# Optimization experiments

Measured on AMD Instinct MI355X. Metric: run time of the kernel, lower is better.

The kernel has to match this reference:

```python
import jax, jax.numpy as jnp
import numpy as np

B, S, E, NH = 2, 2048, 1024, 16
THETA = 10000.0


def setup_inputs() -> dict:
    key = jax.random.key(0)
    k1, k2 = jax.random.split(key, 2)
    hidden_states = jax.random.normal(k1, (B, S, E), dtype=jnp.float32)
    in_proj_weight = jax.random.normal(k2, (3 * E, E), dtype=jnp.float32) * 0.02
    in_proj_bias = jnp.zeros((3 * E,), dtype=jnp.float32)
    return {
        "hidden_states": hidden_states,
        "in_proj_weight": in_proj_weight,
        "in_proj_bias": in_proj_bias,
        "T": 1,
        "H": 32,
        "W": 64,
    }


def _rope(x, cos, sin):
    # x: [BT, seq, n_heads, head_dim]; cos/sin: [seq, head_dim//2]
    # pairs are consecutive elements (x[2i], x[2i+1]) == complex (re, im)
    xr = x.reshape(x.shape[:-1] + (-1, 2))
    xe, xo = xr[..., 0], xr[..., 1]
    c = cos[None, :, None, :]
    s = sin[None, :, None, :]
    re = xe * c - xo * s
    im = xe * s + xo * c
    return jnp.stack([re, im], axis=-1).reshape(x.shape)


def reference(hidden_states, in_proj_weight, in_proj_bias, T, H, W):
    Bx, Sx, Ex = hidden_states.shape
    hd = Ex // NH
    # fused QKV projection
    qkv = hidden_states @ in_proj_weight.T + in_proj_bias
    q, k, v = jnp.split(qkv, 3, axis=-1)
    # 1D rotary over chunks of length S//T (T=1 -> full sequence)
    seq = Sx // T
    inv_freq = 1.0 / (THETA ** (jnp.arange(0, hd, 2, dtype=jnp.float32) / hd))
    ang = jnp.arange(seq, dtype=jnp.float32)[:, None] * inv_freq  # [seq, hd//2]
    cos, sin = jnp.cos(ang), jnp.sin(ang)
    q = _rope(q.reshape(Bx * T, seq, NH, hd), cos, sin).reshape(Bx, Sx, NH, hd)
    k = _rope(k.reshape(Bx * T, seq, NH, hd), cos, sin).reshape(Bx, Sx, NH, hd)
    v = v.reshape(Bx, Sx, NH, hd)
    # scaled dot-product attention (special_attn encoder path: no out_proj)
    scale = 1.0 / jnp.sqrt(jnp.asarray(hd, dtype=jnp.float32))
    scores = jnp.einsum('bqnd,bknd->bnqk', q, k) * scale
    attn = jax.nn.softmax(scores, axis=-1)
    out = jnp.einsum('bnqk,bknd->bqnd', attn, v)
    return out.reshape(Bx, Sx, Ex)
```

## Files before the change

kernel.cpp:

```cpp
#include <hip/hip_runtime.h>
#include <math.h>

#define BB 2
#define SS 2048
#define EE 1024
#define NHH 16
#define HD 64
#define HD2 32

typedef _Float16 f16x8 __attribute__((ext_vector_type(8)));
typedef __attribute__((ext_vector_type(4))) float f32x4;

static __device__ __forceinline__ unsigned pkh(float a, float b) {
    union { _Float16 h[2]; unsigned u; } v;
    v.h[0] = (_Float16)a; v.h[1] = (_Float16)b;
    return v.u;
}

static __device__ __forceinline__ void dma16(const void* g, void* l) {
    __builtin_amdgcn_global_load_lds(
        (const __attribute__((address_space(1))) unsigned int*)g,
        (__attribute__((address_space(3))) unsigned int*)l,
        16, 0, 0);
}

__global__ __launch_bounds__(256) void rope_table_k(float* __restrict__ ct,
                                                    float* __restrict__ st) {
    int idx = blockIdx.x * 256 + threadIdx.x;
    if (idx >= SS * HD2) return;
    int s = idx >> 5, p = idx & 31;
    double inv = pow(10000.0, -(double)(2 * p) / 64.0);
    double ang = (double)s * inv;
    ct[idx] = (float)cos(ang);
    st[idx] = (float)sin(ang);
}

#define NXCHUNK 524288
#define NWCHUNK 393216
__global__ __launch_bounds__(256) void cvt_k(
    const float* __restrict__ X, const float* __restrict__ W,
    unsigned short* __restrict__ Xh, unsigned short* __restrict__ Wh)
{
    int idx = blockIdx.x * 256 + threadIdx.x;
    const float* src;
    unsigned short* dst;
    int c;
    if (idx < NXCHUNK) { src = X; dst = Xh; c = idx; }
    else               { src = W; dst = Wh; c = idx - NXCHUNK;
                         if (c >= NWCHUNK) return; }
    int l15 = c & 15, q = (c >> 4) & 3, grp = (c >> 6) & 7;
    int kt = (c >> 9) & 31, t = c >> 14;
    int row = t * 128 + grp * 16 + l15;
    int k   = kt * 32 + q * 8;
    float4 v0 = *(const float4*)(src + (size_t)row * EE + k);
    float4 v1 = *(const float4*)(src + (size_t)row * EE + k + 4);
    *(uint4*)(dst + (size_t)c * 8) =
        make_uint4(pkh(v0.x, v0.y), pkh(v0.z, v0.w), pkh(v1.x, v1.y), pkh(v1.z, v1.w));
}

__global__ __launch_bounds__(256, 3) void qkv_mfma_k(
    const unsigned short* __restrict__ Xh, const unsigned short* __restrict__ Wh,
    const float* __restrict__ bias,
    const float* __restrict__ ct, const float* __restrict__ st,
    unsigned short* __restrict__ Qg, unsigned short* __restrict__ Kg,
    unsigned short* __restrict__ Vg)
{
    __shared__ __align__(16) unsigned short Alds[4096];
    __shared__ __align__(16) unsigned short Blds[4096];

    const int tid  = threadIdx.x;
    const int wave = tid >> 6;
    const int lane = tid & 63;
    const int quad = lane >> 4;
    const int l15  = lane & 15;

    const int id    = blockIdx.x;
    const int xcd   = id & 7;
    const int local = id >> 3;
    const int nt    = xcd * 3 + local % 3;
    const int mt    = local / 3;
    const int m0    = mt * 128;
    const int n0b   = nt * 128;

    f32x4 acc[4][4];
#pragma unroll
    for (int mc = 0; mc < 4; mc++)
#pragma unroll
        for (int nc = 0; nc < 4; nc++) acc[mc][nc] = (f32x4){0.f, 0.f, 0.f, 0.f};

    const int mg = (wave >> 1) * 4;
    const int ng = (wave & 1) * 4;

    for (int kt = 0; kt < EE / 32; kt++) {
        __syncthreads();
        {
            const unsigned short* at = Xh + ((size_t)(mt * 32 + kt)) * 4096;
            const unsigned short* bt = Wh + ((size_t)(nt * 32 + kt)) * 4096;
            dma16(at + (size_t)tid * 8,         Alds + tid * 8);
            dma16(at + (size_t)(tid + 256) * 8, Alds + (tid + 256) * 8);
            dma16(bt + (size_t)tid * 8,         Blds + tid * 8);
            dma16(bt + (size_t)(tid + 256) * 8, Blds + (tid + 256) * 8);
        }
        __syncthreads();

        f16x8 Af[4], Bf[4];
#pragma unroll
        for (int mc = 0; mc < 4; mc++)
            Af[mc] = *(const f16x8*)(Alds + ((mg + mc) * 4 + quad) * 128 + l15 * 8);
#pragma unroll
        for (int nc = 0; nc < 4; nc++)
            Bf[nc] = *(const f16x8*)(Blds + ((ng + nc) * 4 + quad) * 128 + l15 * 8);
#pragma unroll
        for (int mc = 0; mc < 4; mc++)
#pragma unroll
            for (int nc = 0; nc < 4; nc++)
                acc[mc][nc] = __builtin_amdgcn_mfma_f32_16x16x32_f16(Af[mc], Bf[nc], acc[mc][nc], 0, 0, 0);
    }

    const int n0w = n0b + (wave & 1) * 64;
    const int m0w = m0 + (wave >> 1) * 64;
    const int sec = n0w >> 10;
    const int h   = (n0w & 1023) >> 6;
    const int bq  = m0w >> 11;
    const size_t abase = (size_t)(bq * NHH + h) * 131072;
    unsigned short* dst = (sec == 0) ? Qg : (sec == 1) ? Kg : Vg;

    float bn[4];
#pragma unroll
    for (int nc = 0; nc < 4; nc++) bn[nc] = bias[n0w + nc * 16 + l15];

    if (sec < 2) {
        const float scq = (sec == 0) ? 0.18033688f : 1.0f;
#pragma unroll
        for (int mc = 0; mc < 4; mc++) {
            int sb = (m0w & 2047) + mc * 16;
#pragma unroll
            for (int nc = 0; nc < 4; nc++) {
                int d = nc * 16 + l15;
                int p = d >> 1;
                int kc_d = d >> 5, quad_a = (d >> 3) & 3, j = d & 7;
#pragma unroll
                for (int rr = 0; rr < 4; rr++) {
                    int srow = sb + quad * 4 + rr;
                    float x = acc[mc][nc][rr] + bn[nc];
                    float xp = __shfl_xor(x, 1);
                    float c = ct[srow * 32 + p], sn = st[srow * 32 + p];
                    float o = ((l15 & 1) == 0) ? (x * c - xp * sn) : (xp * sn + x * c);
                    o *= scq;
                    float op = __shfl_xor(o, 1);
                    if ((l15 & 1) == 0) {
                        unsigned u = pkh(o, op);
                        size_t e = abase +
                            (size_t)((((srow >> 4) * 2 + kc_d) * 4 + quad_a)) * 128 +
                            (srow & 15) * 8 + j;
                        *(unsigned int*)(dst + e) = u;
                    }
                }
            }
        }
    } else {
#pragma unroll
        for (int mc = 0; mc < 4; mc++) {
            int sb = (m0w & 2047) + mc * 16;
            int s32 = sb >> 5;
            int quad_v = ((sb >> 3) + (quad >> 1)) & 3;
            int j0 = (quad & 1) * 4;
#pragma unroll
            for (int nc = 0; nc < 4; nc++) {
                float x0 = acc[mc][nc][0] + bn[nc];
                float x1 = acc[mc][nc][1] + bn[nc];
                float x2 = acc[mc][nc][2] + bn[nc];
                float x3 = acc[mc][nc][3] + bn[nc];
                unsigned u01 = pkh(x0, x1), u23 = pkh(x2, x3);
                size_t e = abase +
                    (size_t)(((s32 * 4 + nc) * 4 + quad_v)) * 128 + l15 * 8 + j0;
                *(uint2*)(dst + e) = make_uint2(u01, u23);
            }
        }
    }
}

__global__ __launch_bounds__(256, 4) void attn_mfma_k(
    const unsigned short* __restrict__ Qg,
    const unsigned short* __restrict__ Kg,
    const unsigned short* __restrict__ Vg,
    float* __restrict__ out)
{
    __shared__ __align__(16) unsigned short Klds[2][4096];
    __shared__ __align__(16) unsigned short Pbuf[4][1024];

    const int tid  = threadIdx.x;
    const int wave = tid >> 6;
    const int lane = tid & 63;
    const int quad = lane >> 4;
    const int l15  = lane & 15;
    const int id   = blockIdx.x;
    const int bh   = (id & 7) * 4 + ((id >> 3) & 3);
    const int qt   = id >> 5;
    const int b    = bh >> 4, h = bh & 15;
    const int q0   = qt * 64 + wave * 16;
    const size_t abase = (size_t)bh * 131072;

    f16x8 qf[2];
#pragma unroll
    for (int kc = 0; kc < 2; kc++)
        qf[kc] = *(const f16x8*)(Qg + abase +
            (size_t)((((q0 >> 4) * 2 + kc) * 4 + quad)) * 128 + l15 * 8);

    f32x4 acc[4];
#pragma unroll
    for (int dc = 0; dc < 4; dc++) acc[dc] = (f32x4){0.f, 0.f, 0.f, 0.f};
    float mst = -INFINITY, lst = 0.f;

    const unsigned short* kgb = Kg + abase;
    const unsigned short* vgb = Vg + abase;
    unsigned short* Pw = Pbuf[wave];

    dma16(kgb + (size_t)tid * 8,         &Klds[0][tid * 8]);
    dma16(kgb + (size_t)(tid + 256) * 8, &Klds[0][(tid + 256) * 8]);
    __syncthreads();

    int cur = 0;
    for (int kt = 0; kt < SS / 64; kt++) {
        if (kt + 1 < SS / 64) {
            const unsigned short* ks = kgb + (size_t)(kt + 1) * 4096;
            dma16(ks + (size_t)tid * 8,         &Klds[cur ^ 1][tid * 8]);
            dma16(ks + (size_t)(tid + 256) * 8, &Klds[cur ^ 1][(tid + 256) * 8]);
        }

        const unsigned short* vt = vgb + (size_t)kt * 4096;
        f16x8 vf[4][2];
#pragma unroll
        for (int dc = 0; dc < 4; dc++)
#pragma unroll
            for (int kk2 = 0; kk2 < 2; kk2++)
                vf[dc][kk2] = *(const f16x8*)(vt + (kk2 * 16 + dc * 4 + quad) * 128 + l15 * 8);

        f32x4 stt[4];
        __builtin_amdgcn_s_setprio(1);
#pragma unroll
        for (int mc = 0; mc < 4; mc++) {
            f16x8 a0 = *(const f16x8*)(&Klds[cur][((mc * 2 + 0) * 4 + quad) * 128 + l15 * 8]);
            f16x8 a1 = *(const f16x8*)(&Klds[cur][((mc * 2 + 1) * 4 + quad) * 128 + l15 * 8]);
            f32x4 s = (f32x4){0.f, 0.f, 0.f, 0.f};
            s = __builtin_amdgcn_mfma_f32_16x16x32_f16(a0, qf[0], s, 0, 0, 0);
            s = __builtin_amdgcn_mfma_f32_16x16x32_f16(a1, qf[1], s, 0, 0, 0);
            stt[mc] = s;
        }
        __builtin_amdgcn_s_setprio(0);

        float mt = -INFINITY;
#pragma unroll
        for (int mc = 0; mc < 4; mc++)
#pragma unroll
            for (int rr = 0; rr < 4; rr++) mt = fmaxf(mt, stt[mc][rr]);
        mt = fmaxf(mt, __shfl_xor(mt, 16));
        mt = fmaxf(mt, __shfl_xor(mt, 32));

        if (!__all(mt - mst <= 8.f)) {
            float mnew = fmaxf(mst, mt);
            float alpha = __builtin_amdgcn_exp2f(mst - mnew);
            lst *= alpha;
            float ar[4];
#pragma unroll
            for (int rr = 0; rr < 4; rr++)
                ar[rr] = __shfl(alpha, (lane & 48) + ((lane >> 4) << 2) + rr);
#pragma unroll
            for (int dc = 0; dc < 4; dc++)
#pragma unroll
                for (int rr = 0; rr < 4; rr++) acc[dc][rr] *= ar[rr];
            mst = mnew;
        }

        float ps = 0.f;
#pragma unroll
        for (int mc = 0; mc < 4; mc++) {
            float e0 = __builtin_amdgcn_exp2f(stt[mc][0] - mst);
            float e1 = __builtin_amdgcn_exp2f(stt[mc][1] - mst);
            float e2 = __builtin_amdgcn_exp2f(stt[mc][2] - mst);
            float e3 = __builtin_amdgcn_exp2f(stt[mc][3] - mst);
            ps += (e0 + e1) + (e2 + e3);
            int kk2 = mc >> 1;
            int quadp = (mc & 1) * 2 + (quad >> 1);
            int j0 = (quad & 1) * 4;
            *(uint2*)(Pw + (kk2 * 4 + quadp) * 128 + l15 * 8 + j0) =
                make_uint2(pkh(e0, e1), pkh(e2, e3));
        }
        ps += __shfl_xor(ps, 16);
        ps += __shfl_xor(ps, 32);
        lst += ps;

        f16x8 pf[2];
#pragma unroll
        for (int kk2 = 0; kk2 < 2; kk2++)
            pf[kk2] = *(const f16x8*)(Pw + (kk2 * 4 + quad) * 128 + l15 * 8);

        __builtin_amdgcn_s_setprio(1);
#pragma unroll
        for (int dc = 0; dc < 4; dc++) {
            f32x4 aa = acc[dc];
#pragma unroll
            for (int kk2 = 0; kk2 < 2; kk2++)
                aa = __builtin_amdgcn_mfma_f32_16x16x32_f16(pf[kk2], vf[dc][kk2], aa, 0, 0, 0);
            acc[dc] = aa;
        }
        __builtin_amdgcn_s_setprio(0);

        __syncthreads();
        cur ^= 1;
    }

    float linv = 1.f / lst;
    float lr[4];
#pragma unroll
    for (int rr = 0; rr < 4; rr++)
        lr[rr] = __shfl(linv, (lane & 48) + ((lane >> 4) << 2) + rr);
#pragma unroll
    for (int dc = 0; dc < 4; dc++)
#pragma unroll
        for (int rr = 0; rr < 4; rr++) {
            int s = q0 + quad * 4 + rr;
            out[((size_t)(b * SS + s)) * EE + h * HD + dc * 16 + l15] = acc[dc][rr] * lr[rr];
        }
}

extern "C" void kernel_launch(void* const* d_in, const int* in_sizes, int n_in,
                              void* d_out, int out_size, void* d_ws, size_t ws_size,
                              hipStream_t stream) {
    const float* X    = (const float*)d_in[0];
    const float* W    = (const float*)d_in[1];
    const float* bias = (const float*)d_in[2];
    float* out = (float*)d_out;

    float* ws = (float*)d_ws;
    float* ct = ws;
    float* st = ws + 65536;
    unsigned short* base = (unsigned short*)(ws + 131072);
    const size_t ASZ = (size_t)32 * 131072;
    unsigned short* Qg = base;
    unsigned short* Kg = base + ASZ;
    unsigned short* Vg = base + 2 * ASZ;
    unsigned short* Xh = base + 3 * ASZ;
    unsigned short* Wh = Xh + (size_t)NXCHUNK * 8;

    rope_table_k<<<(SS * HD2 + 255) / 256, 256, 0, stream>>>(ct, st);
    cvt_k<<<(NXCHUNK + NWCHUNK) / 256, 256, 0, stream>>>(X, W, Xh, Wh);
    qkv_mfma_k<<<dim3(768), 256, 0, stream>>>(
        Xh, Wh, bias, ct, st, Qg, Kg, Vg);
    attn_mfma_k<<<dim3(1024), 256, 0, stream>>>(Qg, Kg, Vg, out);
}
```

Measured before the change: 188.9 us.

## Double-buffer QKV GEMM LDS loads and merge rope-table and convert kernels

The QKV GEMM now double-buffers its A/B LDS tiles. The next k-tile's DMA is issued before the current tile's MFMAs, and one barrier per iteration replaces two, so global loads overlap compute. The rope table and fp16 conversion kernels are merged into one launch, removing one kernel launch. The attention kernel's V and K address arithmetic is simplified with precomputed lane offsets and incrementing pointers. LDS use in the GEMM doubles to 32 KB per block, which may affect occupancy under the 3-blocks-per-CU launch bound.

```diff
diff --git a/kernel.cpp b/kernel.cpp
--- a/kernel.cpp
+++ b/kernel.cpp
@@ -24,24 +24,24 @@
         16, 0, 0);
 }
 
-__global__ __launch_bounds__(256) void rope_table_k(float* __restrict__ ct,
-                                                    float* __restrict__ st) {
-    int idx = blockIdx.x * 256 + threadIdx.x;
-    if (idx >= SS * HD2) return;
-    int s = idx >> 5, p = idx & 31;
-    double inv = pow(10000.0, -(double)(2 * p) / 64.0);
-    double ang = (double)s * inv;
-    ct[idx] = (float)cos(ang);
-    st[idx] = (float)sin(ang);
-}
-
 #define NXCHUNK 524288
 #define NWCHUNK 393216
-__global__ __launch_bounds__(256) void cvt_k(
+__global__ __launch_bounds__(256) void tabcvt_k(
     const float* __restrict__ X, const float* __restrict__ W,
-    unsigned short* __restrict__ Xh, unsigned short* __restrict__ Wh)
+    unsigned short* __restrict__ Xh, unsigned short* __restrict__ Wh,
+    float* __restrict__ ct, float* __restrict__ st)
 {
-    int idx = blockIdx.x * 256 + threadIdx.x;
+    int bid = blockIdx.x;
+    if (bid < 256) {
+        int idx = bid * 256 + threadIdx.x;
+        int s = idx >> 5, p = idx & 31;
+        double inv = pow(10000.0, -(double)(2 * p) / 64.0);
+        double ang = (double)s * inv;
+        ct[idx] = (float)cos(ang);
+        st[idx] = (float)sin(ang);
+        return;
+    }
+    int idx = (bid - 256) * 256 + threadIdx.x;
     const float* src;
     unsigned short* dst;
     int c;
@@ -65,8 +65,8 @@
     unsigned short* __restrict__ Qg, unsigned short* __restrict__ Kg,
     unsigned short* __restrict__ Vg)
 {
-    __shared__ __align__(16) unsigned short Alds[4096];
-    __shared__ __align__(16) unsigned short Blds[4096];
+    __shared__ __align__(16) unsigned short Alds[2][4096];
+    __shared__ __align__(16) unsigned short Blds[2][4096];
 
     const int tid  = threadIdx.x;
     const int wave = tid >> 6;
@@ -91,30 +91,42 @@
     const int mg = (wave >> 1) * 4;
     const int ng = (wave & 1) * 4;
 
+    {
+        const unsigned short* at = Xh + ((size_t)(mt * 32)) * 4096;
+        const unsigned short* bt = Wh + ((size_t)(nt * 32)) * 4096;
+        dma16(at + (size_t)tid * 8,         &Alds[0][tid * 8]);
+        dma16(at + (size_t)(tid + 256) * 8, &Alds[0][(tid + 256) * 8]);
+        dma16(bt + (size_t)tid * 8,         &Blds[0][tid * 8]);
+        dma16(bt + (size_t)(tid + 256) * 8, &Blds[0][(tid + 256) * 8]);
+    }
+    __syncthreads();
+
+    int cur = 0;
     for (int kt = 0; kt < EE / 32; kt++) {
-        __syncthreads();
-        {
-            const unsigned short* at = Xh + ((size_t)(mt * 32 + kt)) * 4096;
-            const unsigned short* bt = Wh + ((size_t)(nt * 32 + kt)) * 4096;
-            dma16(at + (size_t)tid * 8,         Alds + tid * 8);
-            dma16(at + (size_t)(tid + 256) * 8, Alds + (tid + 256) * 8);
-            dma16(bt + (size_t)tid * 8,         Blds + tid * 8);
-            dma16(bt + (size_t)(tid + 256) * 8, Blds + (tid + 256) * 8);
-        }
-        __syncthreads();
+        if (kt + 1 < EE / 32) {
+            const unsigned short* at = Xh + ((size_t)(mt * 32 + kt + 1)) * 4096;
+            const unsigned short* bt = Wh + ((size_t)(nt * 32 + kt + 1)) * 4096;
+            dma16(at + (size_t)tid * 8,         &Alds[cur ^ 1][tid * 8]);
+            dma16(at + (size_t)(tid + 256) * 8, &Alds[cur ^ 1][(tid + 256) * 8]);
+            dma16(bt + (size_t)tid * 8,         &Blds[cur ^ 1][tid * 8]);
+            dma16(bt + (size_t)(tid + 256) * 8, &Blds[cur ^ 1][(tid + 256) * 8]);
+        }
 
         f16x8 Af[4], Bf[4];
 #pragma unroll
         for (int mc = 0; mc < 4; mc++)
-            Af[mc] = *(const f16x8*)(Alds + ((mg + mc) * 4 + quad) * 128 + l15 * 8);
+            Af[mc] = *(const f16x8*)(&Alds[cur][((mg + mc) * 4 + quad) * 128 + l15 * 8]);
 #pragma unroll
         for (int nc = 0; nc < 4; nc++)
-            Bf[nc] = *(const f16x8*)(Blds + ((ng + nc) * 4 + quad) * 128 + l15 * 8);
+            Bf[nc] = *(const f16x8*)(&Blds[cur][((ng + nc) * 4 + quad) * 128 + l15 * 8]);
 #pragma unroll
         for (int mc = 0; mc < 4; mc++)
 #pragma unroll
             for (int nc = 0; nc < 4; nc++)
                 acc[mc][nc] = __builtin_amdgcn_mfma_f32_16x16x32_f16(Af[mc], Bf[nc], acc[mc][nc], 0, 0, 0);
+
+        __syncthreads();
+        cur ^= 1;
     }
 
     const int n0w = n0b + (wave & 1) * 64;
@@ -212,8 +224,10 @@
     for (int dc = 0; dc < 4; dc++) acc[dc] = (f32x4){0.f, 0.f, 0.f, 0.f};
     float mst = -INFINITY, lst = 0.f;
 
+    const int laneoff = quad * 128 + l15 * 8;
     const unsigned short* kgb = Kg + abase;
-    const unsigned short* vgb = Vg + abase;
+    const unsigned short* vt0 = Vg + abase + laneoff;
+    const unsigned short* vt1 = vt0 + 2048;
     unsigned short* Pw = Pbuf[wave];
 
     dma16(kgb + (size_t)tid * 8,         &Klds[0][tid * 8]);
@@ -228,20 +242,20 @@
             dma16(ks + (size_t)(tid + 256) * 8, &Klds[cur ^ 1][(tid + 256) * 8]);
         }
 
-        const unsigned short* vt = vgb + (size_t)kt * 4096;
         f16x8 vf[4][2];
 #pragma unroll
-        for (int dc = 0; dc < 4; dc++)
-#pragma unroll
-            for (int kk2 = 0; kk2 < 2; kk2++)
-                vf[dc][kk2] = *(const f16x8*)(vt + (kk2 * 16 + dc * 4 + quad) * 128 + l15 * 8);
-
+        for (int dc = 0; dc < 4; dc++) {
+            vf[dc][0] = *(const f16x8*)(vt0 + dc * 512);
+            vf[dc][1] = *(const f16x8*)(vt1 + dc * 512);
+        }
+
+        const unsigned short* kb = &Klds[cur][laneoff];
         f32x4 stt[4];
         __builtin_amdgcn_s_setprio(1);
 #pragma unroll
         for (int mc = 0; mc < 4; mc++) {
-            f16x8 a0 = *(const f16x8*)(&Klds[cur][((mc * 2 + 0) * 4 + quad) * 128 + l15 * 8]);
-            f16x8 a1 = *(const f16x8*)(&Klds[cur][((mc * 2 + 1) * 4 + quad) * 128 + l15 * 8]);
+            f16x8 a0 = *(const f16x8*)(kb + mc * 1024);
+            f16x8 a1 = *(const f16x8*)(kb + mc * 1024 + 512);
             f32x4 s = (f32x4){0.f, 0.f, 0.f, 0.f};
             s = __builtin_amdgcn_mfma_f32_16x16x32_f16(a0, qf[0], s, 0, 0, 0);
             s = __builtin_amdgcn_mfma_f32_16x16x32_f16(a1, qf[1], s, 0, 0, 0);
@@ -308,6 +322,8 @@
 
         __syncthreads();
         cur ^= 1;
+        vt0 += 4096;
+        vt1 += 4096;
     }
 
     float linv = 1.f / lst;
@@ -343,8 +359,8 @@
     unsigned short* Xh = base + 3 * ASZ;
     unsigned short* Wh = Xh + (size_t)NXCHUNK * 8;
 
-    rope_table_k<<<(SS * HD2 + 255) / 256, 256, 0, stream>>>(ct, st);
-    cvt_k<<<(NXCHUNK + NWCHUNK) / 256, 256, 0, stream>>>(X, W, Xh, Wh);
+    tabcvt_k<<<dim3(256 + (NXCHUNK + NWCHUNK) / 256), 256, 0, stream>>>(
+        X, W, Xh, Wh, ct, st);
     qkv_mfma_k<<<dim3(768), 256, 0, stream>>>(
         Xh, Wh, bias, ct, st, Qg, Kg, Vg);
     attn_mfma_k<<<dim3(1024), 256, 0, stream>>>(Qg, Kg, Vg, out);
```

After: 185.9 us. About the same (-1.5%).
